# Optimization experiments

Hardware: AMD Instinct MI355X
Metric: run time of the kernel (lower is better)

The kernel has to match this reference:

```python
import jax, jax.numpy as jnp
import numpy as np

# Static module configuration (matches init_kwargs)
B, C_IN, H, W = 128, 64, 32, 32
C_OUT = 128
K = 3
PAD = 1
STRIDE = 1
OUT_H = (H + 2 * PAD - K) // STRIDE + 1  # 32
OUT_W = (W + 2 * PAD - K) // STRIDE + 1  # 32
L = OUT_H * OUT_W                        # 1024
IN_FEAT = C_IN * K * K                   # 576


def setup_inputs() -> dict:
    key = jax.random.key(0)
    k1, k2, k3 = jax.random.split(key, 3)
    x = jax.random.normal(k1, (B, C_IN, H, W), dtype=jnp.float32)
    # kaiming-uniform-ish scale: 1/sqrt(fan_in)
    bound = 1.0 / np.sqrt(IN_FEAT)
    weight = jax.random.uniform(k2, (L, IN_FEAT, C_OUT), dtype=jnp.float32,
                                minval=-bound, maxval=bound)
    bias = jax.random.uniform(k3, (L, C_OUT), dtype=jnp.float32,
                              minval=-bound, maxval=bound)
    return {"x": x, "weight": weight, "bias": bias}


def _unfold(x):
    """torch.nn.Unfold equivalent: returns (B, L, C*K*K), channel-major feature order."""
    xp = jnp.pad(x, ((0, 0), (0, 0), (PAD, PAD), (PAD, PAD)))
    cols = []
    for i in range(K):
        for j in range(K):
            cols.append(xp[:, :, i:i + OUT_H * STRIDE:STRIDE,
                               j:j + OUT_W * STRIDE:STRIDE])
    # (B, C, K*K, out_h, out_w) -> feature index = c*K*K + i*K + j (torch unfold order)
    p = jnp.stack(cols, axis=2)
    p = p.reshape(x.shape[0], C_IN * K * K, L)
    return p.transpose(0, 2, 1)  # (B, L, in_feat)


def reference(x, weight, bias):
    patches = _unfold(x)                                  # (B, L, in_feat)
    out = jnp.einsum('bli,lio->blo', patches, weight)     # per-location matmul
    out = out + bias[None]                                # (B, L, out_ch)
    out = out.transpose(0, 2, 1).reshape(x.shape[0], C_OUT, OUT_H, OUT_W)
    out = jax.nn.relu(out)
    # MaxPool2d(2, 2)
    Bn = out.shape[0]
    out = out.reshape(Bn, C_OUT, OUT_H // 2, 2, OUT_W // 2, 2).max(axis=(3, 5))
    return out
```

## Files before the change

### kernel.cpp

```cpp
#include <hip/hip_runtime.h>

#define BB   128
#define CI   64
#define HH   32
#define WW   32
#define CO   128
#define IF   576
#define OW   32
#define XH   34
#define XW   34
#define XP_CB    (CI*BB)
#define XP_ELEMS ((size_t)XH*XW*CI*BB)
#define BK   32
#define NIT  72
#define LDK  40

using short8 = __attribute__((ext_vector_type(8))) short;
using f32x4  = __attribute__((ext_vector_type(4))) float;

__device__ __forceinline__ unsigned short f2bf(float f) {
  union { float f; unsigned int u; } v; v.f = f;
  unsigned int u = v.u;
  u = (u + 0x7FFFu + ((u >> 16) & 1u)) >> 16;
  return (unsigned short)u;
}

__global__ __launch_bounds__(256) void transpose_x(
    const float* __restrict__ x, unsigned short* __restrict__ xp) {
  const int c = blockIdx.x >> 5;
  const int h = blockIdx.x & 31;
  __shared__ __align__(16) unsigned short tile[32][136];
  const int t = threadIdx.x;
  const int w = t & 31, b0 = t >> 5;
#pragma unroll
  for (int p = 0; p < 16; ++p) {
    int b = b0 + p * 8;
    float v = x[(((size_t)b * CI + c) * HH + h) * WW + w];
    tile[w][b] = f2bf(v);
  }
  __syncthreads();
  const int w2 = t >> 3;
  const int bb = (t & 7) * 16;
  const unsigned short* src = &tile[w2][bb];
  unsigned short* dst = xp + ((size_t)(h + 1) * XW + (w2 + 1)) * XP_CB + c * BB + bb;
  *(uint4*)(dst)     = *(const uint4*)(src);
  *(uint4*)(dst + 8) = *(const uint4*)(src + 8);
}

__global__ __launch_bounds__(256, 1) void local_gemm_pool(
    const float* __restrict__ Wt, const float* __restrict__ bias,
    const unsigned short* __restrict__ xp, float* __restrict__ out) {
  __shared__ __align__(16) unsigned short Asl[3][BB][LDK];
  __shared__ __align__(16) unsigned short Bsl[3][CO][LDK];
  __shared__ int offs[IF];

  const int tid  = threadIdx.x;
  const int lane = tid & 63;
  const int wave = tid >> 6;

  for (int kk = tid; kk < IF; kk += 256) {
    int c = kk / 9, r = kk % 9, di = r / 3, dj = r % 3;
    offs[kk] = ((di * XW + dj) * CI + c) * BB;
  }

  const int bidx = blockIdx.x;
  const int x8 = bidx & 7, j = bidx >> 3;
  const int ph = 2 * x8 + (j >> 4), pw = j & 15;

  const int sn = tid & 127;
  const int kh = tid >> 7;

  const int r16 = lane & 15;
  const int q8  = (lane >> 4) * 8;
  const int m0  = (wave >> 1) * 64;
  const int n0  = (wave & 1) * 64;

  f32x4 acc[4][4] = {};
  f32x4 rmx[4][4] = {};

  float          breg0[16], breg1[16];
  unsigned short areg0[16], areg1[16];

  __syncthreads();

  auto issue = [&](int it, float* br, unsigned short* ar) {
    const int loc = it / 18, kc = it % 18, k0 = kc * BK;
    const int oh = 2 * ph + (loc >> 1), ow = 2 * pw + (loc & 1);
    const int l  = oh * OW + ow;
    const float* wp = Wt + ((size_t)l * IF + (k0 + kh * 16)) * CO + sn;
#pragma unroll
    for (int i = 0; i < 16; ++i) br[i] = wp[(size_t)i * CO];
    const int base = (oh * XW + ow) * XP_CB + sn;
#pragma unroll
    for (int i = 0; i < 16; ++i) ar[i] = xp[base + offs[k0 + kh * 16 + i]];
  };

  auto writeLds = [&](int it, const float* br, const unsigned short* ar) {
    const int bufI = it % 3;
    const int col  = kh * 16;
#pragma unroll
    for (int p = 0; p < 2; ++p) {
      short8 vb, va;
#pragma unroll
      for (int i = 0; i < 8; ++i) {
        vb[i] = (short)f2bf(br[p * 8 + i]);
        va[i] = (short)ar[p * 8 + i];
      }
      *(short8*)&Bsl[bufI][sn][col + p * 8] = vb;
      *(short8*)&Asl[bufI][sn][col + p * 8] = va;
    }
  };

  auto computeChunk = [&](int it) {
    const int bufI = it % 3;
    short8 af[4], bf[4];
#pragma unroll
    for (int tm = 0; tm < 4; ++tm)
      af[tm] = *(const short8*)&Asl[bufI][m0 + tm * 16 + r16][q8];
#pragma unroll
    for (int tn = 0; tn < 4; ++tn)
      bf[tn] = *(const short8*)&Bsl[bufI][n0 + tn * 16 + r16][q8];
#pragma unroll
    for (int tm = 0; tm < 4; ++tm)
#pragma unroll
      for (int tn = 0; tn < 4; ++tn)
        acc[tm][tn] = __builtin_amdgcn_mfma_f32_16x16x32_bf16(
            af[tm], bf[tn], acc[tm][tn], 0, 0, 0);
  };

  auto finishLoc = [&](int loc) {
    const int oh = 2 * ph + (loc >> 1), ow = 2 * pw + (loc & 1);
    const int l  = oh * OW + ow;
#pragma unroll
    for (int tn = 0; tn < 4; ++tn) {
      float bv = bias[l * CO + n0 + tn * 16 + r16];
#pragma unroll
      for (int tm = 0; tm < 4; ++tm)
#pragma unroll
        for (int e = 0; e < 4; ++e) {
          float v = acc[tm][tn][e] + bv;
          v = v > 0.f ? v : 0.f;
          rmx[tm][tn][e] = fmaxf(rmx[tm][tn][e], v);
          acc[tm][tn][e] = 0.f;
        }
    }
  };

  issue(0, breg0, areg0);
  issue(1, breg1, areg1);
  writeLds(0, breg0, areg0);
  issue(2, breg0, areg0);
  writeLds(1, breg1, areg1);
  __syncthreads();

  for (int it2 = 0; it2 < NIT; it2 += 2) {
    if (it2 + 3 < NIT) issue(it2 + 3, breg1, areg1);
    computeChunk(it2);
    if (it2 + 2 < NIT) writeLds(it2 + 2, breg0, areg0);
    __syncthreads();
    const int ito = it2 + 1;
    if (ito + 3 < NIT) issue(ito + 3, breg0, areg0);
    computeChunk(ito);
    if (ito + 2 < NIT) writeLds(ito + 2, breg1, areg1);
    if (ito % 18 == 17) finishLoc(ito / 18);
    __syncthreads();
  }

  float* op = out + (ph * 16 + pw);
#pragma unroll
  for (int tm = 0; tm < 4; ++tm)
#pragma unroll
    for (int e = 0; e < 4; ++e) {
      const int row = m0 + tm * 16 + (lane >> 4) * 4 + e;
#pragma unroll
      for (int tn = 0; tn < 4; ++tn) {
        const int col = n0 + tn * 16 + r16;
        op[((size_t)row * CO + col) * 256] = rmx[tm][tn][e];
      }
    }
}

extern "C" void kernel_launch(void* const* d_in, const int* in_sizes, int n_in,
                              void* d_out, int out_size, void* d_ws, size_t ws_size,
                              hipStream_t stream) {
  (void)in_sizes; (void)n_in; (void)out_size; (void)ws_size;
  const float* x  = (const float*)d_in[0];
  const float* w  = (const float*)d_in[1];
  const float* bs = (const float*)d_in[2];
  float* out = (float*)d_out;
  unsigned short* xp = (unsigned short*)d_ws;

  hipMemsetAsync(xp, 0, XP_ELEMS * sizeof(unsigned short), stream);
  transpose_x<<<dim3(CI * HH), dim3(256), 0, stream>>>(x, xp);
  local_gemm_pool<<<dim3(256), dim3(256), 0, stream>>>(w, bs, xp, out);
}
```

Before: 479.0 us.

## Split output channels across two blocks with 512-thread blocks and double buffering

Each block now computes half of the output channels (64) for its pooled position, doubling the grid to 512 blocks, and uses 512 threads (8 waves) with one 16-wide N tile per wave. The LDS pipeline drops from triple to double buffering, and per-thread register staging shrinks, with launch bounds raised to allow more resident blocks. The aim is to fill more CUs and raise occupancy so the memory-bound weight stream is spread more widely. The trade-off is that the im2col A tile is now loaded twice (once per channel half), each wave gets less MFMA reuse per A fragment, and prefetch depth is lower.

```diff
diff --git a/kernel.cpp b/kernel.cpp
--- a/kernel.cpp
+++ b/kernel.cpp
@@ -14,8 +14,10 @@
 #define BK   32
 #define NIT  72
 #define LDK  40
+#define COB  64
 
 using short8 = __attribute__((ext_vector_type(8))) short;
+using bf16x4 = __attribute__((ext_vector_type(4))) short;
 using f32x4  = __attribute__((ext_vector_type(4))) float;
 
 __device__ __forceinline__ unsigned short f2bf(float f) {
@@ -47,39 +49,44 @@
   *(uint4*)(dst + 8) = *(const uint4*)(src + 8);
 }
 
-__global__ __launch_bounds__(256, 1) void local_gemm_pool(
+__global__ __launch_bounds__(512, 4) void local_gemm_pool(
     const float* __restrict__ Wt, const float* __restrict__ bias,
     const unsigned short* __restrict__ xp, float* __restrict__ out) {
-  __shared__ __align__(16) unsigned short Asl[3][BB][LDK];
-  __shared__ __align__(16) unsigned short Bsl[3][CO][LDK];
+  __shared__ __align__(16) unsigned short Asl[2][BB][LDK];
+  __shared__ __align__(16) unsigned short Bsl[2][COB][LDK];
   __shared__ int offs[IF];
 
   const int tid  = threadIdx.x;
   const int lane = tid & 63;
   const int wave = tid >> 6;
 
-  for (int kk = tid; kk < IF; kk += 256) {
+  for (int kk = tid; kk < IF; kk += 512) {
     int c = kk / 9, r = kk % 9, di = r / 3, dj = r % 3;
     offs[kk] = ((di * XW + dj) * CI + c) * BB;
   }
 
   const int bidx = blockIdx.x;
   const int x8 = bidx & 7, j = bidx >> 3;
-  const int ph = 2 * x8 + (j >> 4), pw = j & 15;
+  const int coh = j & 1;
+  const int pw  = (j >> 1) & 15;
+  const int ph  = 2 * x8 + (j >> 5);
+  const int co0 = coh * COB;
 
-  const int sn = tid & 127;
-  const int kh = tid >> 7;
+  const int sa = tid & 127;
+  const int ka = tid >> 7;
+  const int sb = tid & 63;
+  const int kb = tid >> 6;
 
   const int r16 = lane & 15;
   const int q8  = (lane >> 4) * 8;
-  const int m0  = (wave >> 1) * 64;
-  const int n0  = (wave & 1) * 64;
+  const int m0  = (wave >> 2) * 64;
+  const int n0  = (wave & 3) * 16;
 
-  f32x4 acc[4][4] = {};
-  f32x4 rmx[4][4] = {};
+  f32x4 acc[4] = {};
+  f32x4 rmx[4] = {};
 
-  float          breg0[16], breg1[16];
-  unsigned short areg0[16], areg1[16];
+  float          breg0[4], breg1[4];
+  unsigned short areg0[8], areg1[8];
 
   __syncthreads();
 
@@ -87,96 +94,79 @@
     const int loc = it / 18, kc = it % 18, k0 = kc * BK;
     const int oh = 2 * ph + (loc >> 1), ow = 2 * pw + (loc & 1);
     const int l  = oh * OW + ow;
-    const float* wp = Wt + ((size_t)l * IF + (k0 + kh * 16)) * CO + sn;
+    const float* wp = Wt + ((size_t)l * IF + (k0 + kb * 4)) * CO + co0 + sb;
 #pragma unroll
-    for (int i = 0; i < 16; ++i) br[i] = wp[(size_t)i * CO];
-    const int base = (oh * XW + ow) * XP_CB + sn;
+    for (int i = 0; i < 4; ++i) br[i] = wp[(size_t)i * CO];
+    const int base = (oh * XW + ow) * XP_CB + sa;
 #pragma unroll
-    for (int i = 0; i < 16; ++i) ar[i] = xp[base + offs[k0 + kh * 16 + i]];
+    for (int i = 0; i < 8; ++i) ar[i] = xp[base + offs[k0 + ka * 8 + i]];
   };
 
   auto writeLds = [&](int it, const float* br, const unsigned short* ar) {
-    const int bufI = it % 3;
-    const int col  = kh * 16;
+    const int bufI = it & 1;
+    bf16x4 vb;
 #pragma unroll
-    for (int p = 0; p < 2; ++p) {
-      short8 vb, va;
+    for (int i = 0; i < 4; ++i) vb[i] = (short)f2bf(br[i]);
+    *(bf16x4*)&Bsl[bufI][sb][kb * 4] = vb;
+    short8 va;
 #pragma unroll
-      for (int i = 0; i < 8; ++i) {
-        vb[i] = (short)f2bf(br[p * 8 + i]);
-        va[i] = (short)ar[p * 8 + i];
-      }
-      *(short8*)&Bsl[bufI][sn][col + p * 8] = vb;
-      *(short8*)&Asl[bufI][sn][col + p * 8] = va;
-    }
+    for (int i = 0; i < 8; ++i) va[i] = (short)ar[i];
+    *(short8*)&Asl[bufI][sa][ka * 8] = va;
   };
 
   auto computeChunk = [&](int it) {
-    const int bufI = it % 3;
-    short8 af[4], bf[4];
+    const int bufI = it & 1;
+    short8 af[4], bf;
 #pragma unroll
     for (int tm = 0; tm < 4; ++tm)
       af[tm] = *(const short8*)&Asl[bufI][m0 + tm * 16 + r16][q8];
-#pragma unroll
-    for (int tn = 0; tn < 4; ++tn)
-      bf[tn] = *(const short8*)&Bsl[bufI][n0 + tn * 16 + r16][q8];
+    bf = *(const short8*)&Bsl[bufI][n0 + r16][q8];
 #pragma unroll
     for (int tm = 0; tm < 4; ++tm)
-#pragma unroll
-      for (int tn = 0; tn < 4; ++tn)
-        acc[tm][tn] = __builtin_amdgcn_mfma_f32_16x16x32_bf16(
-            af[tm], bf[tn], acc[tm][tn], 0, 0, 0);
+      acc[tm] = __builtin_amdgcn_mfma_f32_16x16x32_bf16(af[tm], bf, acc[tm], 0, 0, 0);
   };
 
   auto finishLoc = [&](int loc) {
     const int oh = 2 * ph + (loc >> 1), ow = 2 * pw + (loc & 1);
     const int l  = oh * OW + ow;
+    const float bv = bias[l * CO + co0 + n0 + r16];
 #pragma unroll
-    for (int tn = 0; tn < 4; ++tn) {
-      float bv = bias[l * CO + n0 + tn * 16 + r16];
+    for (int tm = 0; tm < 4; ++tm)
 #pragma unroll
-      for (int tm = 0; tm < 4; ++tm)
-#pragma unroll
-        for (int e = 0; e < 4; ++e) {
-          float v = acc[tm][tn][e] + bv;
-          v = v > 0.f ? v : 0.f;
-          rmx[tm][tn][e] = fmaxf(rmx[tm][tn][e], v);
-          acc[tm][tn][e] = 0.f;
-        }
-    }
+      for (int e = 0; e < 4; ++e) {
+        float v = acc[tm][e] + bv;
+        v = v > 0.f ? v : 0.f;
+        rmx[tm][e] = fmaxf(rmx[tm][e], v);
+        acc[tm][e] = 0.f;
+      }
   };
 
   issue(0, breg0, areg0);
   issue(1, breg1, areg1);
   writeLds(0, breg0, areg0);
-  issue(2, breg0, areg0);
-  writeLds(1, breg1, areg1);
   __syncthreads();
 
   for (int it2 = 0; it2 < NIT; it2 += 2) {
-    if (it2 + 3 < NIT) issue(it2 + 3, breg1, areg1);
+    if (it2 + 2 < NIT) issue(it2 + 2, breg0, areg0);
     computeChunk(it2);
-    if (it2 + 2 < NIT) writeLds(it2 + 2, breg0, areg0);
+    writeLds(it2 + 1, breg1, areg1);
     __syncthreads();
     const int ito = it2 + 1;
-    if (ito + 3 < NIT) issue(ito + 3, breg0, areg0);
+    if (ito + 2 < NIT) issue(ito + 2, breg1, areg1);
     computeChunk(ito);
-    if (ito + 2 < NIT) writeLds(ito + 2, breg1, areg1);
+    if (ito + 1 < NIT) writeLds(ito + 1, breg0, areg0);
     if (ito % 18 == 17) finishLoc(ito / 18);
     __syncthreads();
   }
 
   float* op = out + (ph * 16 + pw);
+  const int col = co0 + n0 + r16;
 #pragma unroll
   for (int tm = 0; tm < 4; ++tm)
 #pragma unroll
     for (int e = 0; e < 4; ++e) {
       const int row = m0 + tm * 16 + (lane >> 4) * 4 + e;
-#pragma unroll
-      for (int tn = 0; tn < 4; ++tn) {
-        const int col = n0 + tn * 16 + r16;
-        op[((size_t)row * CO + col) * 256] = rmx[tm][tn][e];
-      }
+      op[((size_t)row * CO + col) * 256] = rmx[tm][e];
     }
 }
 
@@ -192,5 +182,5 @@
 
   hipMemsetAsync(xp, 0, XP_ELEMS * sizeof(unsigned short), stream);
   transpose_x<<<dim3(CI * HH), dim3(256), 0, stream>>>(x, xp);
-  local_gemm_pool<<<dim3(256), dim3(256), 0, stream>>>(w, bs, xp, out);
+  local_gemm_pool<<<dim3(512), dim3(512), 0, stream>>>(w, bs, xp, out);
 }
```

Result: faster. 460.8 us (-3.8%).
